# Kernel tuning notes

Measured on AMD Instinct MI355X. Metric: run time of the kernel, lower is better.

The kernel has to match this reference:

```python
import jax, jax.numpy as jnp
import numpy as np

L, B, N, D, H, DH, DFF = 12, 4, 512, 768, 12, 64, 3072
SCALE = 1.0 / np.sqrt(DH).astype(np.float32)


def _ln(x, s, b):
    m = x.mean(-1, keepdims=True)
    v = ((x - m) ** 2).mean(-1, keepdims=True)
    return (x - m) * jax.lax.rsqrt(v + 1e-5) * s + b


def setup_inputs() -> dict:
    key = jax.random.key(0)
    ks = jax.random.split(key, 6)
    w = 0.02
    return {
        "x": jax.random.normal(ks[0], (B, N, D), jnp.float32),
        "ln1_s": jnp.ones((L, D), jnp.float32),
        "ln1_b": jnp.zeros((L, D), jnp.float32),
        "wqkv": jax.random.normal(ks[1], (L, D, 3 * H * DH), jnp.float32) * w,
        "wo": jax.random.normal(ks[2], (L, H * DH, D), jnp.float32) * w,
        "bo": jnp.zeros((L, D), jnp.float32),
        "ln2_s": jnp.ones((L, D), jnp.float32),
        "ln2_b": jnp.zeros((L, D), jnp.float32),
        "w1": jax.random.normal(ks[3], (L, D, DFF), jnp.float32) * w,
        "b1": jnp.zeros((L, DFF), jnp.float32),
        "w2": jax.random.normal(ks[4], (L, DFF, D), jnp.float32) * w,
        "b2": jnp.zeros((L, D), jnp.float32),
    }


def reference(x, ln1_s, ln1_b, wqkv, wo, bo, ln2_s, ln2_b, w1, b1, w2, b2):
    b, n, d = x.shape

    def layer(x, p):
        l1s, l1b, qkv_w, wo_, bo_, l2s, l2b, w1_, b1_, w2_, b2_ = p
        # --- pre-norm multi-head self-attention (softmax) ---
        h = _ln(x, l1s, l1b)
        qkv = h @ qkv_w                              # [b, n, 3*H*DH]
        q, k, v = jnp.split(qkv, 3, axis=-1)
        def heads(t):                                # [b, n, H*DH] -> [b, H, n, DH]
            return t.reshape(b, n, H, DH).transpose(0, 2, 1, 3)
        q, k, v = heads(q), heads(k), heads(v)
        scores = jnp.einsum("bhnd,bhmd->bhnm", q, k) * SCALE
        attn = jax.nn.softmax(scores, axis=-1)       # [b, H, n, n]
        o = jnp.einsum("bhnm,bhmd->bhnd", attn, v)
        o = o.transpose(0, 2, 1, 3).reshape(b, n, H * DH)
        x = x + (o @ wo_ + bo_)                      # residual 1 (dropout p=0)
        # --- pre-norm feed-forward (GELU, exact erf as in torch) ---
        h2 = _ln(x, l2s, l2b)
        ff = jax.nn.gelu(h2 @ w1_ + b1_, approximate=False) @ w2_ + b2_
        x = x + ff                                   # residual 2
        return x, attn

    out, weights = jax.lax.scan(
        layer, x, (ln1_s, ln1_b, wqkv, wo, bo, ln2_s, ln2_b, w1, b1, w2, b2)
    )
    return out, weights  # weights: [L, b, H, n, n], matching the per-layer list
```

## Files before the change

### kernel.cpp

```cpp
#include <hip/hip_runtime.h>
#include <hip/hip_bf16.h>

typedef __hip_bfloat16 bf16;
typedef float f32x4 __attribute__((ext_vector_type(4)));
typedef __bf16 b16x8 __attribute__((ext_vector_type(8)));

constexpr int Lc = 12, Bc = 4, Nc = 512, Dc = 768, Hc = 12, DHc = 64, DFFc = 3072;
constexpr int QKVc = 3 * Dc;
constexpr int Mrows = Bc * Nc;
constexpr float SCALE = 0.125f;

__device__ __forceinline__ bf16 f2b(float x) { return __float2bfloat16(x); }

__device__ __forceinline__ void mfma_bf16(f32x4& d, b16x8 a, b16x8 b) {
  d = __builtin_amdgcn_mfma_f32_16x16x32_bf16(a, b, d, 0, 0, 0);
}

__device__ __forceinline__ void gload16(const bf16* g, bf16* l) {
  __builtin_amdgcn_global_load_lds(
      (const __attribute__((address_space(1))) void*)g,
      (__attribute__((address_space(3))) void*)l, 16, 0, 0);
}

template <int BM, int BN, int WM, int WN, int MODE, int SPLITK = 1>
__global__ __launch_bounds__(256) void gemm_bt(
    const bf16* __restrict__ Abase, const bf16* __restrict__ Btbase,
    const float* __restrict__ bias, float* __restrict__ xres,
    bf16* __restrict__ outb, bf16* __restrict__ vtout,
    int M, int N, int K, int lda, int ldb, int ldc) {
  constexpr int MI = WM / 16, NI = WN / 16;
  constexpr int NWN = BN / WN;
  const int tid = threadIdx.x;
  const int lane = tid & 63, wave = tid >> 6;
  const int wm = (wave / NWN) * WM, wn = (wave % NWN) * WN;
  const int tm0 = blockIdx.x * BM, tn0 = blockIdx.y * BN;
  const int z = blockIdx.z;

  const bf16* A = Abase;
  const bf16* Bt = Btbase;

  const int Kslice = K / SPLITK;
  const int kbase = (SPLITK > 1) ? z * Kslice : 0;

  __shared__ __align__(16) bf16 As[2][BM * 64];
  __shared__ __align__(16) bf16 Bs[2][BN * 64];

  f32x4 acc[MI][NI] = {};

  const int nt = Kslice >> 6;

  auto stage = [&](int buf, int k0) {
    #pragma unroll
    for (int rr = 0; rr < BM / 32; rr++) {
      int idx = rr * 256 + tid;
      int row = idx >> 3, c8 = idx & 7;
      int sc = ((c8 ^ (row & 7)) << 3);
      gload16(A + (size_t)(tm0 + row) * lda + (kbase + k0 + sc), &As[buf][idx * 8]);
    }
    #pragma unroll
    for (int rr = 0; rr < BN / 32; rr++) {
      int idx = rr * 256 + tid;
      int row = idx >> 3, c8 = idx & 7;
      int sc = ((c8 ^ (row & 7)) << 3);
      gload16(Bt + (size_t)(tn0 + row) * ldb + (kbase + k0 + sc), &Bs[buf][idx * 8]);
    }
  };

  stage(0, 0);
  __syncthreads();

  int cur = 0;
  for (int kt = 0; kt < nt; kt++) {
    if (kt + 1 < nt) stage(cur ^ 1, (kt + 1) * 64);

    b16x8 af[2][MI], bfr[2][NI];
    #pragma unroll
    for (int ks = 0; ks < 2; ks++) {
      #pragma unroll
      for (int i = 0; i < MI; i++) {
        int r = wm + i * 16 + (lane & 15);
        int c = ks * 4 + (lane >> 4);
        af[ks][i] = *(const b16x8*)(&As[cur][r * 64 + ((c ^ (r & 7)) << 3)]);
      }
      #pragma unroll
      for (int j = 0; j < NI; j++) {
        int r = wn + j * 16 + (lane & 15);
        int c = ks * 4 + (lane >> 4);
        bfr[ks][j] = *(const b16x8*)(&Bs[cur][r * 64 + ((c ^ (r & 7)) << 3)]);
      }
    }
    #pragma unroll
    for (int ks = 0; ks < 2; ks++)
      #pragma unroll
      for (int i = 0; i < MI; i++)
        #pragma unroll
        for (int j = 0; j < NI; j++)
          mfma_bf16(acc[i][j], af[ks][i], bfr[ks][j]);

    __syncthreads();
    cur ^= 1;
  }

  const int r0 = (lane >> 4) * 4;
  const int c0 = lane & 15;
  #pragma unroll
  for (int i = 0; i < MI; i++) {
    #pragma unroll
    for (int j = 0; j < NI; j++) {
      #pragma unroll
      for (int r = 0; r < 4; r++) {
        int row = tm0 + wm + i * 16 + r0 + r;
        int col = tn0 + wn + j * 16 + c0;
        float v = acc[i][j][r];
        if (MODE == 0) {
          bf16 bv = f2b(v);
          outb[(size_t)row * ldc + col] = bv;
          if (col >= 2 * Dc) {
            int cv = col - 2 * Dc;
            int bh = (row >> 9) * Hc + (cv >> 6);
            vtout[((size_t)bh * DHc + (cv & 63)) * Nc + (row & 511)] = bv;
          }
        } else if (MODE == 1) {
          v += bias[col];
          float g = 0.5f * v * (1.0f + erff(v * 0.70710678118654752f));
          outb[(size_t)row * ldc + col] = f2b(g);
        } else if (MODE == 2) {
          if (SPLITK > 1) {
            if (z == 0) v += bias[col];
            atomicAdd(&xres[(size_t)row * ldc + col], v);
          } else {
            v += bias[col];
            xres[(size_t)row * ldc + col] += v;
          }
        }
      }
    }
  }
}

__global__ __launch_bounds__(256) void fattn_k(const bf16* __restrict__ qkv,
                                               const bf16* __restrict__ vt,
                                               float* __restrict__ attn_f,
                                               bf16* __restrict__ o) {
  const int bh = blockIdx.y;
  const int b = bh / Hc, h = bh % Hc;
  const int n0 = blockIdx.x * 32;
  const int tid = threadIdx.x, lane = tid & 63, wave = tid >> 6;
  const int wn = wave * 128;

  __shared__ __align__(16) bf16 P[32 * 512];
  __shared__ float red[32][4];

  const bf16* qbase = qkv + (size_t)b * Nc * QKVc + h * DHc;
  const bf16* kbase = qbase + Dc;
  const bf16* vthead = vt + (size_t)bh * DHc * Nc;

  b16x8 qf[2][2];
  #pragma unroll
  for (int ks = 0; ks < 2; ks++)
    #pragma unroll
    for (int i = 0; i < 2; i++)
      qf[ks][i] = *(const b16x8*)(qbase +
          (size_t)(n0 + i * 16 + (lane & 15)) * QKVc + ks * 32 + (lane >> 4) * 8);

  f32x4 acc[2][8] = {};
  #pragma unroll
  for (int ks = 0; ks < 2; ks++) {
    #pragma unroll
    for (int j = 0; j < 8; j++) {
      b16x8 kf = *(const b16x8*)(kbase +
          (size_t)(wn + j * 16 + (lane & 15)) * QKVc + ks * 32 + (lane >> 4) * 8);
      #pragma unroll
      for (int i = 0; i < 2; i++)
        mfma_bf16(acc[i][j], qf[ks][i], kf);
    }
  }

  #pragma unroll
  for (int i = 0; i < 2; i++)
    #pragma unroll
    for (int j = 0; j < 8; j++)
      acc[i][j] *= SCALE;

  const int r0 = (lane >> 4) * 4, c0 = lane & 15;
  float rmax[2][4];
  #pragma unroll
  for (int i = 0; i < 2; i++)
    #pragma unroll
    for (int rr = 0; rr < 4; rr++) {
      float m = -1e30f;
      #pragma unroll
      for (int j = 0; j < 8; j++) m = fmaxf(m, acc[i][j][rr]);
      #pragma unroll
      for (int of = 1; of < 16; of <<= 1) m = fmaxf(m, __shfl_xor(m, of));
      rmax[i][rr] = m;
    }
  if (c0 == 0) {
    #pragma unroll
    for (int i = 0; i < 2; i++)
      #pragma unroll
      for (int rr = 0; rr < 4; rr++)
        red[i * 16 + r0 + rr][wave] = rmax[i][rr];
  }
  __syncthreads();
  #pragma unroll
  for (int i = 0; i < 2; i++)
    #pragma unroll
    for (int rr = 0; rr < 4; rr++) {
      int r = i * 16 + r0 + rr;
      rmax[i][rr] = fmaxf(fmaxf(red[r][0], red[r][1]), fmaxf(red[r][2], red[r][3]));
    }
  __syncthreads();

  float rsum[2][4];
  #pragma unroll
  for (int i = 0; i < 2; i++)
    #pragma unroll
    for (int rr = 0; rr < 4; rr++) {
      float s = 0.f;
      #pragma unroll
      for (int j = 0; j < 8; j++) {
        float e = expf(acc[i][j][rr] - rmax[i][rr]);
        acc[i][j][rr] = e;
        s += e;
      }
      #pragma unroll
      for (int of = 1; of < 16; of <<= 1) s += __shfl_xor(s, of);
      rsum[i][rr] = s;
    }
  if (c0 == 0) {
    #pragma unroll
    for (int i = 0; i < 2; i++)
      #pragma unroll
      for (int rr = 0; rr < 4; rr++)
        red[i * 16 + r0 + rr][wave] = rsum[i][rr];
  }
  __syncthreads();
  #pragma unroll
  for (int i = 0; i < 2; i++)
    #pragma unroll
    for (int rr = 0; rr < 4; rr++) {
      int r = i * 16 + r0 + rr;
      rsum[i][rr] = 1.0f / (red[r][0] + red[r][1] + red[r][2] + red[r][3]);
    }

  float* of32 = attn_f + (size_t)bh * Nc * Nc;
  #pragma unroll
  for (int i = 0; i < 2; i++)
    #pragma unroll
    for (int j = 0; j < 8; j++)
      #pragma unroll
      for (int rr = 0; rr < 4; rr++) {
        int rloc = i * 16 + r0 + rr;
        int col = wn + j * 16 + c0;
        float p = acc[i][j][rr] * rsum[i][rr];
        of32[(size_t)(n0 + rloc) * Nc + col] = p;
        P[rloc * 512 + (col ^ ((rloc & 7) << 3))] = f2b(p);
      }
  __syncthreads();

  f32x4 oacc[2] = {};
  const int dd = wave * 16 + (lane & 15);
  #pragma unroll
  for (int ks = 0; ks < 16; ks++) {
    int kvb = ks * 32 + ((lane >> 4) << 3);
    b16x8 bf_ = *(const b16x8*)(vthead + (size_t)dd * 512 + kvb);
    #pragma unroll
    for (int i = 0; i < 2; i++) {
      int q = i * 16 + (lane & 15);
      b16x8 af_ = *(const b16x8*)(P + q * 512 + (kvb ^ ((q & 7) << 3)));
      mfma_bf16(oacc[i], af_, bf_);
    }
  }
  #pragma unroll
  for (int i = 0; i < 2; i++)
    #pragma unroll
    for (int r = 0; r < 4; r++) {
      int row = b * Nc + n0 + i * 16 + r0 + r;
      o[(size_t)row * Dc + h * DHc + wave * 16 + c0] = f2b(oacc[i][r]);
    }
}

__global__ __launch_bounds__(256) void lntwb_k(
    const float* __restrict__ x, const float* __restrict__ s,
    const float* __restrict__ b, bf16* __restrict__ out,
    const float* __restrict__ wqkv_l, const float* __restrict__ wo_l,
    const float* __restrict__ w1_l, const float* __restrict__ w2_l,
    bf16* __restrict__ wTq, bf16* __restrict__ wTo,
    bf16* __restrict__ wT1, bf16* __restrict__ wT2) {
  __shared__ bf16 t[64][65];
  const int tid = threadIdx.x;
  if (blockIdx.x < 2048) {
    const int row = blockIdx.x;
    const float* xr = x + (size_t)row * Dc;
    float a0 = xr[tid], a1 = xr[tid + 256], a2 = xr[tid + 512];
    float sum = a0 + a1 + a2;
    float sq = a0 * a0 + a1 * a1 + a2 * a2;
    #pragma unroll
    for (int o = 32; o; o >>= 1) {
      sum += __shfl_down(sum, o);
      sq += __shfl_down(sq, o);
    }
    float* s1 = (float*)t;
    float* s2 = s1 + 4;
    if ((tid & 63) == 0) { s1[tid >> 6] = sum; s2[tid >> 6] = sq; }
    __syncthreads();
    sum = s1[0] + s1[1] + s1[2] + s1[3];
    sq = s2[0] + s2[1] + s2[2] + s2[3];
    float m = sum * (1.0f / Dc);
    float var = sq * (1.0f / Dc) - m * m;
    float rs = rsqrtf(var + 1e-5f);
    bf16* orow = out + (size_t)row * Dc;
    orow[tid]       = f2b((a0 - m) * rs * s[tid]       + b[tid]);
    orow[tid + 256] = f2b((a1 - m) * rs * s[tid + 256] + b[tid + 256]);
    orow[tid + 512] = f2b((a2 - m) * rs * s[tid + 512] + b[tid + 512]);
    return;
  }
  int f = blockIdx.x - 2048;
  const float* in;
  bf16* outp;
  int K, Nw, n0, k0;
  if (f < 432)       { in = wqkv_l; outp = wTq; K = Dc;   Nw = QKVc; n0 = (f % 36) * 64; k0 = (f / 36) * 64; }
  else if (f < 576)  { f -= 432;  in = wo_l; outp = wTo; K = Dc;   Nw = Dc;   n0 = (f % 12) * 64; k0 = (f / 12) * 64; }
  else if (f < 1152) { f -= 576;  in = w1_l; outp = wT1; K = Dc;   Nw = DFFc; n0 = (f % 48) * 64; k0 = (f / 48) * 64; }
  else               { f -= 1152; in = w2_l; outp = wT2; K = DFFc; Nw = Dc;   n0 = (f % 12) * 64; k0 = (f / 12) * 64; }
  const int tx = tid & 63, ty = tid >> 6;
  #pragma unroll
  for (int kk = ty; kk < 64; kk += 4)
    t[tx][kk] = f2b(in[(size_t)(k0 + kk) * Nw + n0 + tx]);
  __syncthreads();
  #pragma unroll
  for (int nn = ty; nn < 64; nn += 4)
    outp[(size_t)(n0 + nn) * K + k0 + tx] = t[nn][tx];
}

__global__ __launch_bounds__(256) void ln_k(const float* __restrict__ x,
                                            const float* __restrict__ s,
                                            const float* __restrict__ b,
                                            bf16* __restrict__ out) {
  const int row = blockIdx.x, tid = threadIdx.x;
  const float* xr = x + (size_t)row * Dc;
  float a0 = xr[tid], a1 = xr[tid + 256], a2 = xr[tid + 512];
  float sum = a0 + a1 + a2;
  float sq = a0 * a0 + a1 * a1 + a2 * a2;
  #pragma unroll
  for (int o = 32; o; o >>= 1) {
    sum += __shfl_down(sum, o);
    sq += __shfl_down(sq, o);
  }
  __shared__ float s1[4], s2[4];
  if ((tid & 63) == 0) { s1[tid >> 6] = sum; s2[tid >> 6] = sq; }
  __syncthreads();
  sum = s1[0] + s1[1] + s1[2] + s1[3];
  sq = s2[0] + s2[1] + s2[2] + s2[3];
  float m = sum * (1.0f / Dc);
  float var = sq * (1.0f / Dc) - m * m;
  float rs = rsqrtf(var + 1e-5f);
  bf16* orow = out + (size_t)row * Dc;
  orow[tid]       = f2b((a0 - m) * rs * s[tid]       + b[tid]);
  orow[tid + 256] = f2b((a1 - m) * rs * s[tid + 256] + b[tid + 256]);
  orow[tid + 512] = f2b((a2 - m) * rs * s[tid + 512] + b[tid + 512]);
}

extern "C" void kernel_launch(void* const* d_in, const int* in_sizes, int n_in,
                              void* d_out, int out_size, void* d_ws, size_t ws_size,
                              hipStream_t stream) {
  const float* x_in  = (const float*)d_in[0];
  const float* ln1_s = (const float*)d_in[1];
  const float* ln1_b = (const float*)d_in[2];
  const float* wqkv  = (const float*)d_in[3];
  const float* wo    = (const float*)d_in[4];
  const float* bo    = (const float*)d_in[5];
  const float* ln2_s = (const float*)d_in[6];
  const float* ln2_b = (const float*)d_in[7];
  const float* w1    = (const float*)d_in[8];
  const float* b1    = (const float*)d_in[9];
  const float* w2    = (const float*)d_in[10];
  const float* b2    = (const float*)d_in[11];
  float* out = (float*)d_out;

  char* ws = (char*)d_ws;
  float* x      = (float*)(ws + 0);
  bf16* h       = (bf16*)(ws + 6291456);
  bf16* qkv     = (bf16*)(ws + 9437184);
  bf16* o       = (bf16*)(ws + 18874368);
  bf16* ff      = (bf16*)(ws + 22020096);
  bf16* vt      = (bf16*)(ws + 34603008);
  bf16* wTq     = (bf16*)(ws + 37748736);
  bf16* wTo     = (bf16*)(ws + 41287680);
  bf16* wT1     = (bf16*)(ws + 42467328);
  bf16* wT2     = (bf16*)(ws + 47185920);
  if (ws_size < (size_t)51904512) return;

  hipMemcpyAsync(x, x_in, (size_t)Mrows * Dc * sizeof(float),
                 hipMemcpyDeviceToDevice, stream);

  constexpr size_t ATTN_BASE = (size_t)Mrows * Dc;
  constexpr size_t ATTN_L = (size_t)Bc * Hc * Nc * Nc;

  for (int l = 0; l < Lc; l++) {
    float* attn_l = out + ATTN_BASE + (size_t)l * ATTN_L;

    lntwb_k<<<3776, 256, 0, stream>>>(
        x, ln1_s + l * Dc, ln1_b + l * Dc, h,
        wqkv + (size_t)l * Dc * QKVc, wo + (size_t)l * Dc * Dc,
        w1 + (size_t)l * Dc * DFFc, w2 + (size_t)l * DFFc * Dc,
        wTq, wTo, wT1, wT2);

    gemm_bt<128, 128, 64, 64, 0><<<dim3(Mrows / 128, QKVc / 128, 1), 256, 0, stream>>>(
        h, wTq, nullptr, nullptr, qkv, vt, Mrows, QKVc, Dc, Dc, Dc, QKVc);
    fattn_k<<<dim3(Nc / 32, Bc * Hc), 256, 0, stream>>>(qkv, vt, attn_l, o);
    gemm_bt<128, 64, 64, 32, 2, 2><<<dim3(Mrows / 128, Dc / 64, 2), 256, 0, stream>>>(
        o, wTo, bo + l * Dc, x, nullptr, nullptr, Mrows, Dc, Dc, Dc, Dc, Dc);

    ln_k<<<Mrows, 256, 0, stream>>>(x, ln2_s + l * Dc, ln2_b + l * Dc, h);
    gemm_bt<128, 128, 64, 64, 1><<<dim3(Mrows / 128, DFFc / 128, 1), 256, 0, stream>>>(
        h, wT1, b1 + l * DFFc, nullptr, ff, nullptr, Mrows, DFFc, Dc, Dc, Dc, DFFc);
    gemm_bt<128, 64, 64, 32, 2, 4><<<dim3(Mrows / 128, Dc / 64, 4), 256, 0, stream>>>(
        ff, wT2, b2 + l * Dc, x, nullptr, nullptr, Mrows, Dc, DFFc, DFFc, DFFc, Dc);
  }

  hipMemcpyAsync(out, x, (size_t)Mrows * Dc * sizeof(float),
                 hipMemcpyDeviceToDevice, stream);
}
```

Baseline: 1.843 ms.

## Split weight-conversion kernel, shrink GEMM tiles, raise split-K, drop softmax barrier

```diff
diff --git a/kernel.cpp b/kernel.cpp
--- a/kernel.cpp
+++ b/kernel.cpp
@@ -149,7 +149,8 @@
   const int wn = wave * 128;
 
   __shared__ __align__(16) bf16 P[32 * 512];
-  __shared__ float red[32][4];
+  __shared__ float redm[32][4];
+  __shared__ float reds[32][4];
 
   const bf16* qbase = qkv + (size_t)b * Nc * QKVc + h * DHc;
   const bf16* kbase = qbase + Dc;
@@ -200,7 +201,7 @@
     for (int i = 0; i < 2; i++)
       #pragma unroll
       for (int rr = 0; rr < 4; rr++)
-        red[i * 16 + r0 + rr][wave] = rmax[i][rr];
+        redm[i * 16 + r0 + rr][wave] = rmax[i][rr];
   }
   __syncthreads();
   #pragma unroll
@@ -208,9 +209,8 @@
     #pragma unroll
     for (int rr = 0; rr < 4; rr++) {
       int r = i * 16 + r0 + rr;
-      rmax[i][rr] = fmaxf(fmaxf(red[r][0], red[r][1]), fmaxf(red[r][2], red[r][3]));
-    }
-  __syncthreads();
+      rmax[i][rr] = fmaxf(fmaxf(redm[r][0], redm[r][1]), fmaxf(redm[r][2], redm[r][3]));
+    }
 
   float rsum[2][4];
   #pragma unroll
@@ -233,7 +233,7 @@
     for (int i = 0; i < 2; i++)
       #pragma unroll
       for (int rr = 0; rr < 4; rr++)
-        red[i * 16 + r0 + rr][wave] = rsum[i][rr];
+        reds[i * 16 + r0 + rr][wave] = rsum[i][rr];
   }
   __syncthreads();
   #pragma unroll
@@ -241,7 +241,7 @@
     #pragma unroll
     for (int rr = 0; rr < 4; rr++) {
       int r = i * 16 + r0 + rr;
-      rsum[i][rr] = 1.0f / (red[r][0] + red[r][1] + red[r][2] + red[r][3]);
+      rsum[i][rr] = 1.0f / (reds[r][0] + reds[r][1] + reds[r][2] + reds[r][3]);
     }
 
   float* of32 = attn_f + (size_t)bh * Nc * Nc;
@@ -281,49 +281,9 @@
     }
 }
 
-__global__ __launch_bounds__(256) void lntwb_k(
-    const float* __restrict__ x, const float* __restrict__ s,
-    const float* __restrict__ b, bf16* __restrict__ out,
-    const float* __restrict__ wqkv_l, const float* __restrict__ wo_l,
-    const float* __restrict__ w1_l, const float* __restrict__ w2_l,
-    bf16* __restrict__ wTq, bf16* __restrict__ wTo,
-    bf16* __restrict__ wT1, bf16* __restrict__ wT2) {
-  __shared__ bf16 t[64][65];
-  const int tid = threadIdx.x;
-  if (blockIdx.x < 2048) {
-    const int row = blockIdx.x;
-    const float* xr = x + (size_t)row * Dc;
-    float a0 = xr[tid], a1 = xr[tid + 256], a2 = xr[tid + 512];
-    float sum = a0 + a1 + a2;
-    float sq = a0 * a0 + a1 * a1 + a2 * a2;
-    #pragma unroll
-    for (int o = 32; o; o >>= 1) {
-      sum += __shfl_down(sum, o);
-      sq += __shfl_down(sq, o);
-    }
-    float* s1 = (float*)t;
-    float* s2 = s1 + 4;
-    if ((tid & 63) == 0) { s1[tid >> 6] = sum; s2[tid >> 6] = sq; }
-    __syncthreads();
-    sum = s1[0] + s1[1] + s1[2] + s1[3];
-    sq = s2[0] + s2[1] + s2[2] + s2[3];
-    float m = sum * (1.0f / Dc);
-    float var = sq * (1.0f / Dc) - m * m;
-    float rs = rsqrtf(var + 1e-5f);
-    bf16* orow = out + (size_t)row * Dc;
-    orow[tid]       = f2b((a0 - m) * rs * s[tid]       + b[tid]);
-    orow[tid + 256] = f2b((a1 - m) * rs * s[tid + 256] + b[tid + 256]);
-    orow[tid + 512] = f2b((a2 - m) * rs * s[tid + 512] + b[tid + 512]);
-    return;
-  }
-  int f = blockIdx.x - 2048;
-  const float* in;
-  bf16* outp;
-  int K, Nw, n0, k0;
-  if (f < 432)       { in = wqkv_l; outp = wTq; K = Dc;   Nw = QKVc; n0 = (f % 36) * 64; k0 = (f / 36) * 64; }
-  else if (f < 576)  { f -= 432;  in = wo_l; outp = wTo; K = Dc;   Nw = Dc;   n0 = (f % 12) * 64; k0 = (f / 12) * 64; }
-  else if (f < 1152) { f -= 576;  in = w1_l; outp = wT1; K = Dc;   Nw = DFFc; n0 = (f % 48) * 64; k0 = (f / 48) * 64; }
-  else               { f -= 1152; in = w2_l; outp = wT2; K = DFFc; Nw = Dc;   n0 = (f % 12) * 64; k0 = (f / 12) * 64; }
+__device__ __forceinline__ void twb_tile(const float* in, bf16* outp,
+                                         int K, int Nw, int n0, int k0,
+                                         bf16 (*t)[65], int tid) {
   const int tx = tid & 63, ty = tid >> 6;
   #pragma unroll
   for (int kk = ty; kk < 64; kk += 4)
@@ -334,12 +294,9 @@
     outp[(size_t)(n0 + nn) * K + k0 + tx] = t[nn][tx];
 }
 
-__global__ __launch_bounds__(256) void ln_k(const float* __restrict__ x,
-                                            const float* __restrict__ s,
-                                            const float* __restrict__ b,
-                                            bf16* __restrict__ out) {
-  const int row = blockIdx.x, tid = threadIdx.x;
-  const float* xr = x + (size_t)row * Dc;
+__device__ __forceinline__ void ln_row(const float* xr, const float* s,
+                                       const float* b, bf16* orow,
+                                       float* s1, float* s2, int tid) {
   float a0 = xr[tid], a1 = xr[tid + 256], a2 = xr[tid + 512];
   float sum = a0 + a1 + a2;
   float sq = a0 * a0 + a1 * a1 + a2 * a2;
@@ -348,7 +305,6 @@
     sum += __shfl_down(sum, o);
     sq += __shfl_down(sq, o);
   }
-  __shared__ float s1[4], s2[4];
   if ((tid & 63) == 0) { s1[tid >> 6] = sum; s2[tid >> 6] = sq; }
   __syncthreads();
   sum = s1[0] + s1[1] + s1[2] + s1[3];
@@ -356,10 +312,43 @@
   float m = sum * (1.0f / Dc);
   float var = sq * (1.0f / Dc) - m * m;
   float rs = rsqrtf(var + 1e-5f);
-  bf16* orow = out + (size_t)row * Dc;
   orow[tid]       = f2b((a0 - m) * rs * s[tid]       + b[tid]);
   orow[tid + 256] = f2b((a1 - m) * rs * s[tid + 256] + b[tid + 256]);
   orow[tid + 512] = f2b((a2 - m) * rs * s[tid + 512] + b[tid + 512]);
+}
+
+__global__ __launch_bounds__(256) void lntwb1_k(
+    const float* __restrict__ x, const float* __restrict__ s,
+    const float* __restrict__ b, bf16* __restrict__ out,
+    const float* __restrict__ wqkv_l, const float* __restrict__ wo_l,
+    bf16* __restrict__ wTq, bf16* __restrict__ wTo) {
+  __shared__ bf16 t[64][65];
+  const int tid = threadIdx.x;
+  if (blockIdx.x < 2048) {
+    ln_row(x + (size_t)blockIdx.x * Dc, s, b, out + (size_t)blockIdx.x * Dc,
+           (float*)t, (float*)t + 4, tid);
+    return;
+  }
+  int f = blockIdx.x - 2048;
+  if (f < 432) twb_tile(wqkv_l, wTq, Dc, QKVc, (f % 36) * 64, (f / 36) * 64, t, tid);
+  else { f -= 432; twb_tile(wo_l, wTo, Dc, Dc, (f % 12) * 64, (f / 12) * 64, t, tid); }
+}
+
+__global__ __launch_bounds__(256) void lntwb2_k(
+    const float* __restrict__ x, const float* __restrict__ s,
+    const float* __restrict__ b, bf16* __restrict__ out,
+    const float* __restrict__ w1_l, const float* __restrict__ w2_l,
+    bf16* __restrict__ wT1, bf16* __restrict__ wT2) {
+  __shared__ bf16 t[64][65];
+  const int tid = threadIdx.x;
+  if (blockIdx.x < 2048) {
+    ln_row(x + (size_t)blockIdx.x * Dc, s, b, out + (size_t)blockIdx.x * Dc,
+           (float*)t, (float*)t + 4, tid);
+    return;
+  }
+  int f = blockIdx.x - 2048;
+  if (f < 576) twb_tile(w1_l, wT1, Dc, DFFc, (f % 48) * 64, (f / 48) * 64, t, tid);
+  else { f -= 576; twb_tile(w2_l, wT2, DFFc, Dc, (f % 12) * 64, (f / 12) * 64, t, tid); }
 }
 
 extern "C" void kernel_launch(void* const* d_in, const int* in_sizes, int n_in,
@@ -401,22 +390,23 @@
   for (int l = 0; l < Lc; l++) {
     float* attn_l = out + ATTN_BASE + (size_t)l * ATTN_L;
 
-    lntwb_k<<<3776, 256, 0, stream>>>(
+    lntwb1_k<<<2624, 256, 0, stream>>>(
         x, ln1_s + l * Dc, ln1_b + l * Dc, h,
-        wqkv + (size_t)l * Dc * QKVc, wo + (size_t)l * Dc * Dc,
-        w1 + (size_t)l * Dc * DFFc, w2 + (size_t)l * DFFc * Dc,
-        wTq, wTo, wT1, wT2);
-
-    gemm_bt<128, 128, 64, 64, 0><<<dim3(Mrows / 128, QKVc / 128, 1), 256, 0, stream>>>(
+        wqkv + (size_t)l * Dc * QKVc, wo + (size_t)l * Dc * Dc, wTq, wTo);
+
+    gemm_bt<128, 64, 64, 32, 0><<<dim3(Mrows / 128, QKVc / 64, 1), 256, 0, stream>>>(
         h, wTq, nullptr, nullptr, qkv, vt, Mrows, QKVc, Dc, Dc, Dc, QKVc);
     fattn_k<<<dim3(Nc / 32, Bc * Hc), 256, 0, stream>>>(qkv, vt, attn_l, o);
-    gemm_bt<128, 64, 64, 32, 2, 2><<<dim3(Mrows / 128, Dc / 64, 2), 256, 0, stream>>>(
+    gemm_bt<128, 64, 64, 32, 2, 4><<<dim3(Mrows / 128, Dc / 64, 4), 256, 0, stream>>>(
         o, wTo, bo + l * Dc, x, nullptr, nullptr, Mrows, Dc, Dc, Dc, Dc, Dc);
 
-    ln_k<<<Mrows, 256, 0, stream>>>(x, ln2_s + l * Dc, ln2_b + l * Dc, h);
-    gemm_bt<128, 128, 64, 64, 1><<<dim3(Mrows / 128, DFFc / 128, 1), 256, 0, stream>>>(
+    lntwb2_k<<<3200, 256, 0, stream>>>(
+        x, ln2_s + l * Dc, ln2_b + l * Dc, h,
+        w1 + (size_t)l * Dc * DFFc, w2 + (size_t)l * DFFc * Dc, wT1, wT2);
+
+    gemm_bt<128, 64, 64, 32, 1><<<dim3(Mrows / 128, DFFc / 64, 1), 256, 0, stream>>>(
         h, wT1, b1 + l * DFFc, nullptr, ff, nullptr, Mrows, DFFc, Dc, Dc, Dc, DFFc);
-    gemm_bt<128, 64, 64, 32, 2, 4><<<dim3(Mrows / 128, Dc / 64, 4), 256, 0, stream>>>(
+    gemm_bt<128, 64, 64, 32, 2, 8><<<dim3(Mrows / 128, Dc / 64, 8), 256, 0, stream>>>(
         ff, wT2, b2 + l * Dc, x, nullptr, nullptr, Mrows, Dc, DFFc, DFFc, DFFc, Dc);
   }
 
```

Measured after the change: 1.932 ms. +4.8%, slower.
